# Performance work log

Hardware: AMD Instinct MI355X
Metric: run time of the kernel (lower is better)

## Reference

```python
import jax, jax.numpy as jnp
import numpy as np

D_MODEL = 1024
N_HEADS = 16
HEAD_DIM = D_MODEL // N_HEADS


def setup_inputs() -> dict:
    key = jax.random.key(0)
    ks = jax.random.split(key, 5)
    B, T = 4, 2048
    x = jax.random.normal(ks[0], (B, T, D_MODEL), dtype=jnp.float32)
    s_in = 1.0 / np.sqrt(D_MODEL)
    W_qkv = jax.random.normal(ks[1], (D_MODEL, 3 * D_MODEL), dtype=jnp.float32) * s_in
    b_qkv = jnp.zeros((3 * D_MODEL,), dtype=jnp.float32)
    W_proj = jax.random.normal(ks[2], (D_MODEL, D_MODEL), dtype=jnp.float32) * s_in
    b_proj = jnp.zeros((D_MODEL,), dtype=jnp.float32)
    return {"x": x, "W_qkv": W_qkv, "b_qkv": b_qkv, "W_proj": W_proj, "b_proj": b_proj}


def reference(x, W_qkv, b_qkv, W_proj, b_proj):
    B, T, C = x.shape
    qkv = x @ W_qkv + b_qkv                       # [B, T, 3C]
    q, k, v = jnp.split(qkv, 3, axis=-1)
    def heads(t):  # [B, T, C] -> [B, H, T, Dh]
        return t.reshape(B, T, N_HEADS, HEAD_DIM).transpose(0, 2, 1, 3)
    q, k, v = heads(q), heads(k), heads(v)
    scale = 1.0 / np.sqrt(HEAD_DIM)
    att = jnp.einsum('bhqd,bhkd->bhqk', q, k) * scale   # [B, H, T, T]
    causal = jnp.tril(jnp.ones((T, T), dtype=bool))
    att = jnp.where(causal, att, -jnp.inf)
    att = jax.nn.softmax(att, axis=-1)
    out = jnp.einsum('bhqk,bhkd->bhqd', att, v)          # [B, H, T, Dh]
    out = out.transpose(0, 2, 1, 3).reshape(B, T, C)
    return out @ W_proj + b_proj
```

## Files before the change

kernel.cpp:

```cpp
#include <hip/hip_runtime.h>
#include <hip/hip_bf16.h>

#define NH 16
#define HD 64
#define T_SEQ 2048
#define DM 1024

typedef __attribute__((ext_vector_type(8))) short short8;
typedef __attribute__((ext_vector_type(4))) short sh4;
typedef __attribute__((ext_vector_type(4))) float f32x4;
typedef __attribute__((ext_vector_type(16))) float f32x16;
typedef unsigned short ushort;

static __device__ __forceinline__ ushort f2bf(float f) {
    union { float f; unsigned int u; } c; c.f = f;
    unsigned int r = (c.u + 0x7fffu + ((c.u >> 16) & 1u)) >> 16;
    return (ushort)r;
}

static __device__ __forceinline__ void gload16(const ushort* g, ushort* l) {
    __builtin_amdgcn_global_load_lds(
        (const __attribute__((address_space(1))) void*)(const void*)g,
        (__attribute__((address_space(3))) void*)(void*)l, 16, 0, 0);
}

__global__ __launch_bounds__(256) void prep(const float* __restrict__ X,
                                            ushort* __restrict__ Xb,
                                            const float* __restrict__ W,
                                            ushort* __restrict__ Wt) {
    __shared__ float Ts[64][65];
    const int tid = threadIdx.x;
    if (blockIdx.x < 4096) {
        int i = blockIdx.x * 256 + tid;
        const float* s = X + (size_t)i * 8;
        float4 a = *(const float4*)(s);
        float4 b = *(const float4*)(s + 4);
        short8 o;
        o[0] = f2bf(a.x); o[1] = f2bf(a.y); o[2] = f2bf(a.z); o[3] = f2bf(a.w);
        o[4] = f2bf(b.x); o[5] = f2bf(b.y); o[6] = f2bf(b.z); o[7] = f2bf(b.w);
        *(short8*)(Xb + (size_t)i * 8) = o;
    } else {
        const int bid = blockIdx.x - 4096;
        const int N = 3 * DM;
        const int n0 = (bid % 48) * 64, k0 = (bid / 48) * 64;
        const int cg = tid & 15, r4 = tid >> 4;
        #pragma unroll
        for (int i = 0; i < 4; ++i) {
            int r = r4 + i * 16;
            float4 v = *(const float4*)(W + (size_t)(k0 + r) * N + n0 + cg * 4);
            Ts[r][cg * 4 + 0] = v.x; Ts[r][cg * 4 + 1] = v.y;
            Ts[r][cg * 4 + 2] = v.z; Ts[r][cg * 4 + 3] = v.w;
        }
        __syncthreads();
        #pragma unroll
        for (int i = 0; i < 4; ++i) {
            int r = r4 + i * 16;
            sh4 o;
            o[0] = (short)f2bf(Ts[cg * 4 + 0][r]);
            o[1] = (short)f2bf(Ts[cg * 4 + 1][r]);
            o[2] = (short)f2bf(Ts[cg * 4 + 2][r]);
            o[3] = (short)f2bf(Ts[cg * 4 + 3][r]);
            *(sh4*)(Wt + (size_t)(n0 + r) * DM + k0 + cg * 4) = o;
        }
    }
}

__global__ __launch_bounds__(256) void transpose_w(const float* __restrict__ W,
                                                   ushort* __restrict__ Wt, int N) {
    __shared__ float Ts[64][65];
    const int n0 = blockIdx.x * 64, k0 = blockIdx.y * 64;
    const int tid = threadIdx.x;
    const int cg = tid & 15, r4 = tid >> 4;
    #pragma unroll
    for (int i = 0; i < 4; ++i) {
        int r = r4 + i * 16;
        float4 v = *(const float4*)(W + (size_t)(k0 + r) * N + n0 + cg * 4);
        Ts[r][cg * 4 + 0] = v.x; Ts[r][cg * 4 + 1] = v.y;
        Ts[r][cg * 4 + 2] = v.z; Ts[r][cg * 4 + 3] = v.w;
    }
    __syncthreads();
    #pragma unroll
    for (int i = 0; i < 4; ++i) {
        int r = r4 + i * 16;
        sh4 o;
        o[0] = (short)f2bf(Ts[cg * 4 + 0][r]);
        o[1] = (short)f2bf(Ts[cg * 4 + 1][r]);
        o[2] = (short)f2bf(Ts[cg * 4 + 2][r]);
        o[3] = (short)f2bf(Ts[cg * 4 + 3][r]);
        *(sh4*)(Wt + (size_t)(n0 + r) * DM + k0 + cg * 4) = o;
    }
}

static __device__ __forceinline__ void gemm_core(
    const ushort* __restrict__ A, const ushort* __restrict__ Bt,
    ushort* __restrict__ smem, int m0, int n0, f32x4 acc[4][4])
{
    const int tid = threadIdx.x;
    const int wid = tid >> 6, lane = tid & 63;
    const int lr = lane & 15, g = lane >> 4;
    const int wm = wid >> 1, wn = wid & 1;
    const int lrow = lane >> 3, lslot = lane & 7;

    auto stage = [&](int b, int kt) {
        ushort* As = smem + b * 16384;
        ushort* Bs = As + 8192;
        #pragma unroll
        for (int i = 0; i < 4; ++i) {
            const int row = wid * 32 + i * 8 + lrow;
            const int gcol = (lslot ^ (row & 7)) * 8;
            const int ldsoff = (wid * 32 + i * 8) * 64;
            gload16(A  + (size_t)(m0 + row) * DM + kt * 64 + gcol, As + ldsoff);
            gload16(Bt + (size_t)(n0 + row) * DM + kt * 64 + gcol, Bs + ldsoff);
        }
    };

    stage(0, 0);
    #pragma unroll 1
    for (int kt = 0; kt < 16; ++kt) {
        const int cur = kt & 1;
        if (kt < 15) {
            stage(cur ^ 1, kt + 1);
            asm volatile("s_waitcnt vmcnt(8)" ::: "memory");
        } else {
            asm volatile("s_waitcnt vmcnt(0)" ::: "memory");
        }
        __builtin_amdgcn_s_barrier();
        __builtin_amdgcn_sched_barrier(0);
        const ushort* As = smem + cur * 16384;
        const ushort* Bs = As + 8192;
        #pragma unroll
        for (int ks = 0; ks < 2; ++ks) {
            short8 af[4], bfr[4];
            #pragma unroll
            for (int mi = 0; mi < 4; ++mi) {
                int row = wm * 64 + mi * 16 + lr;
                af[mi] = *(const short8*)(As + row * 64 + (((ks * 4 + g) ^ (row & 7)) * 8));
            }
            #pragma unroll
            for (int ni = 0; ni < 4; ++ni) {
                int row = wn * 64 + ni * 16 + lr;
                bfr[ni] = *(const short8*)(Bs + row * 64 + (((ks * 4 + g) ^ (row & 7)) * 8));
            }
            #pragma unroll
            for (int mi = 0; mi < 4; ++mi)
                #pragma unroll
                for (int ni = 0; ni < 4; ++ni)
                    acc[mi][ni] = __builtin_amdgcn_mfma_f32_16x16x32_bf16(af[mi], bfr[ni], acc[mi][ni], 0, 0, 0);
        }
        __builtin_amdgcn_sched_barrier(0);
        __builtin_amdgcn_s_barrier();
    }
}

__global__ __launch_bounds__(256) void qkv_mfma(
    const ushort* __restrict__ Xb, const ushort* __restrict__ Wqt,
    const float* __restrict__ bias,
    ushort* __restrict__ Qb, ushort* __restrict__ Kb, ushort* __restrict__ Vt)
{
    __shared__ __align__(16) ushort smem[32768];
    const int m0 = blockIdx.y * 128;
    const int n0 = blockIdx.x * 128;
    f32x4 acc[4][4] = {};
    gemm_core(Xb, Wqt, smem, m0, n0, acc);

    const int tid = threadIdx.x;
    const int wid = tid >> 6, lane = tid & 63;
    const int lr = lane & 15, g = lane >> 4;
    const int wm = wid >> 1, wn = wid & 1;
    const int which = n0 >> 10;
    const int bq = m0 >> 11;

    if (which < 2) {
        ushort* dst = which ? Kb : Qb;
        const float sc = which ? 1.0f : 0.125f * 1.44269504f;
        #pragma unroll
        for (int ni = 0; ni < 4; ++ni) {
            int nn = n0 + wn * 64 + ni * 16 + lr;
            const float bv = bias[nn];
            const int hh = (nn & 1023) >> 6, dd = nn & 63;
            const size_t hb = ((size_t)(bq * NH + hh)) * T_SEQ;
            #pragma unroll
            for (int mi = 0; mi < 4; ++mi)
                #pragma unroll
                for (int r = 0; r < 4; ++r) {
                    int t = (m0 + wm * 64 + mi * 16 + g * 4 + r) & 2047;
                    dst[(hb + t) * HD + dd] = f2bf((acc[mi][ni][r] + bv) * sc);
                }
        }
    } else {
        __syncthreads();
        ushort* Ct = smem;
        #pragma unroll
        for (int ni = 0; ni < 4; ++ni) {
            int lcol = wn * 64 + ni * 16 + lr;
            const float bv = bias[n0 + lcol];
            #pragma unroll
            for (int mi = 0; mi < 4; ++mi)
                #pragma unroll
                for (int r = 0; r < 4; ++r)
                    Ct[(wm * 64 + mi * 16 + g * 4 + r) * 128 + lcol] = f2bf(acc[mi][ni][r] + bv);
        }
        __syncthreads();
        const int dloc = tid >> 1, th = (tid & 1) * 64;
        const int nn = (n0 & 1023) + dloc;
        ushort* dst = Vt + ((size_t)(bq * 1024 + nn)) * T_SEQ + (m0 & 2047) + th;
        #pragma unroll
        for (int e8 = 0; e8 < 8; ++e8) {
            short8 v;
            #pragma unroll
            for (int u = 0; u < 8; ++u) v[u] = (short)Ct[(th + e8 * 8 + u) * 128 + dloc];
            *(short8*)(dst + e8 * 8) = v;
        }
    }
}

__global__ __launch_bounds__(256) void proj_mfma(
    const ushort* __restrict__ AO, const ushort* __restrict__ Wpt,
    const float* __restrict__ bias, float* __restrict__ Y)
{
    __shared__ __align__(16) ushort smem[32768];
    const int m0 = blockIdx.y * 128;
    const int n0 = blockIdx.x * 128;
    f32x4 acc[4][4] = {};
    gemm_core(AO, Wpt, smem, m0, n0, acc);

    const int tid = threadIdx.x;
    const int wid = tid >> 6, lane = tid & 63;
    const int lr = lane & 15, g = lane >> 4;
    const int wm = wid >> 1, wn = wid & 1;
    #pragma unroll
    for (int ni = 0; ni < 4; ++ni) {
        int nn = n0 + wn * 64 + ni * 16 + lr;
        const float bv = bias[nn];
        #pragma unroll
        for (int mi = 0; mi < 4; ++mi)
            #pragma unroll
            for (int r = 0; r < 4; ++r) {
                int m = m0 + wm * 64 + mi * 16 + g * 4 + r;
                Y[(size_t)m * DM + nn] = acc[mi][ni][r] + bv;
            }
    }
}

__global__ __launch_bounds__(256) void attn_mfma(
    const ushort* __restrict__ Qb,
    const ushort* __restrict__ Kb,
    const ushort* __restrict__ Vt,
    ushort* __restrict__ AO)
{
    __shared__ __align__(16) ushort Ks[2][4096];
    __shared__ __align__(16) ushort Vs[2][4096];

    const int bh = blockIdx.x;
    const int j = 15 - blockIdx.y;
    const int tid = threadIdx.x;
    const int wid = tid >> 6;
    const int lane = tid & 63;
    const int ql = lane & 31;
    const int hi = lane >> 5;

    const ushort* Kg = Kb + (size_t)bh * T_SEQ * HD;
    const ushort* Vg = Vt + (size_t)bh * HD * T_SEQ;

    const int srow = tid >> 3;
    const int sco = (tid & 7) * 8;
    const int ssw = sco ^ ((srow & 7) << 3);
    const int sdst0 = srow * 64 + ssw;
    const int sdst1 = (srow + 32) * 64 + ssw;

    const int b = bh >> 4, h = bh & 15;
    ushort* AOg = AO + (size_t)b * T_SEQ * DM + h * HD;

    const int q0 = j * 128;
    const int qlo = q0 + wid * 32;
    const int ntiles = 2 * j + 2;

    short8 qb[4];
    {
        const ushort* Qg = Qb + ((size_t)bh * T_SEQ + qlo) * HD;
        #pragma unroll
        for (int ds = 0; ds < 4; ++ds)
            qb[ds] = *(const short8*)(Qg + (size_t)ql * HD + ds * 16 + hi * 8);
    }

    f32x16 po[2] = {};
    float lp = 0.f;

    short8 rk0, rk1, rv0, rv1;
    rk0 = *(const short8*)(Kg + (size_t)srow * HD + sco);
    rk1 = *(const short8*)(Kg + (size_t)(srow + 32) * HD + sco);
    rv0 = *(const short8*)(Vg + (size_t)srow * T_SEQ + sco);
    rv1 = *(const short8*)(Vg + (size_t)(srow + 32) * T_SEQ + sco);
    *(short8*)(&Ks[0][sdst0]) = rk0;  *(short8*)(&Ks[0][sdst1]) = rk1;
    *(short8*)(&Vs[0][sdst0]) = rv0;  *(short8*)(&Vs[0][sdst1]) = rv1;
    {
        const int nk0 = 64;
        rk0 = *(const short8*)(Kg + (size_t)(nk0 + srow) * HD + sco);
        rk1 = *(const short8*)(Kg + (size_t)(nk0 + srow + 32) * HD + sco);
        rv0 = *(const short8*)(Vg + (size_t)srow * T_SEQ + nk0 + sco);
        rv1 = *(const short8*)(Vg + (size_t)(srow + 32) * T_SEQ + nk0 + sco);
    }
    __syncthreads();

    for (int tt = 0; tt < ntiles; ++tt) {
        const int k0 = tt * 64;
        const int cur = tt & 1;
        if (tt + 1 < ntiles) {
            const int nxt = cur ^ 1;
            *(short8*)(&Ks[nxt][sdst0]) = rk0;  *(short8*)(&Ks[nxt][sdst1]) = rk1;
            *(short8*)(&Vs[nxt][sdst0]) = rv0;  *(short8*)(&Vs[nxt][sdst1]) = rv1;
            if (tt + 2 < ntiles) {
                const int nk0 = (tt + 2) * 64;
                rk0 = *(const short8*)(Kg + (size_t)(nk0 + srow) * HD + sco);
                rk1 = *(const short8*)(Kg + (size_t)(nk0 + srow + 32) * HD + sco);
                rv0 = *(const short8*)(Vg + (size_t)srow * T_SEQ + nk0 + sco);
                rv1 = *(const short8*)(Vg + (size_t)(srow + 32) * T_SEQ + nk0 + sco);
            }
        }

        if (k0 <= qlo + 31) {
            const ushort* ksb = Ks[cur];
            const ushort* vsb = Vs[cur];

            short8 vf[2][4];
            #pragma unroll
            for (int db = 0; db < 2; ++db)
                #pragma unroll
                for (int sl = 0; sl < 4; ++sl) {
                    int row = db * 32 + ql;
                    int slot = (sl * 2 + hi) ^ (row & 7);
                    vf[db][sl] = *(const short8*)(&vsb[row * 64 + slot * 8]);
                }

            f32x16 sp[2] = {};
            __builtin_amdgcn_s_setprio(1);
            #pragma unroll
            for (int kb = 0; kb < 2; ++kb) {
                #pragma unroll
                for (int ds = 0; ds < 4; ++ds) {
                    int row = kb * 32 + ql;
                    int slot = (ds * 2 + hi) ^ (row & 7);
                    short8 kf = *(const short8*)(&ksb[row * 64 + slot * 8]);
                    sp[kb] = __builtin_amdgcn_mfma_f32_32x32x16_bf16(kf, qb[ds], sp[kb], 0, 0, 0);
                }
            }
            __builtin_amdgcn_s_setprio(0);

            if (k0 + 63 > qlo) {
                #pragma unroll
                for (int kb = 0; kb < 2; ++kb) {
                    const int lim = qlo + ql - k0 - kb * 32 - 4 * hi;
                    #pragma unroll
                    for (int r = 0; r < 16; ++r) {
                        const int c = (r & 3) + 8 * (r >> 2);
                        sp[kb][r] = (c <= lim) ? sp[kb][r] : -INFINITY;
                    }
                }
            }

            float rs = 0.f;
            #pragma unroll
            for (int kb = 0; kb < 2; ++kb)
                #pragma unroll
                for (int r = 0; r < 16; ++r) {
                    float p;
                    asm("v_exp_f32 %0, %1" : "=v"(p) : "v"(sp[kb][r]));
                    sp[kb][r] = p;
                    rs += p;
                }
            lp += rs;

            #pragma unroll
            for (int kb = 0; kb < 2; ++kb) {
                #pragma unroll
                for (int ks16 = 0; ks16 < 2; ++ks16) {
                    unsigned int x0, x1, y0, y1;
                    const int rb0 = ks16 * 2, rb1 = ks16 * 2 + 1;
                    asm("v_cvt_pk_bf16_f32 %0, %1, %2" : "=v"(x0)
                        : "v"(sp[kb][4 * rb0 + 0]), "v"(sp[kb][4 * rb0 + 1]));
                    asm("v_cvt_pk_bf16_f32 %0, %1, %2" : "=v"(x1)
                        : "v"(sp[kb][4 * rb0 + 2]), "v"(sp[kb][4 * rb0 + 3]));
                    asm("v_cvt_pk_bf16_f32 %0, %1, %2" : "=v"(y0)
                        : "v"(sp[kb][4 * rb1 + 0]), "v"(sp[kb][4 * rb1 + 1]));
                    asm("v_cvt_pk_bf16_f32 %0, %1, %2" : "=v"(y1)
                        : "v"(sp[kb][4 * rb1 + 2]), "v"(sp[kb][4 * rb1 + 3]));
                    asm("v_permlane32_swap_b32 %0, %1" : "+v"(x0), "+v"(y0));
                    asm("v_permlane32_swap_b32 %0, %1" : "+v"(x1), "+v"(y1));
                    union { unsigned int w[4]; short8 s8; } pb;
                    pb.w[0] = x0; pb.w[1] = x1; pb.w[2] = y0; pb.w[3] = y1;
                    const int sl = kb * 2 + ks16;
                    __builtin_amdgcn_s_setprio(1);
                    po[0] = __builtin_amdgcn_mfma_f32_32x32x16_bf16(vf[0][sl], pb.s8, po[0], 0, 0, 0);
                    po[1] = __builtin_amdgcn_mfma_f32_32x32x16_bf16(vf[1][sl], pb.s8, po[1], 0, 0, 0);
                    __builtin_amdgcn_s_setprio(0);
                }
            }
        }
        __syncthreads();
    }

    lp += __shfl_xor(lp, 32);
    const float inv = 1.f / lp;
    const int q = qlo + ql;
    #pragma unroll
    for (int db = 0; db < 2; ++db) {
        #pragma unroll
        for (int rb = 0; rb < 4; ++rb) {
            unsigned int w0, w1;
            float f0 = po[db][4 * rb + 0] * inv, f1 = po[db][4 * rb + 1] * inv;
            float f2 = po[db][4 * rb + 2] * inv, f3 = po[db][4 * rb + 3] * inv;
            asm("v_cvt_pk_bf16_f32 %0, %1, %2" : "=v"(w0) : "v"(f0), "v"(f1));
            asm("v_cvt_pk_bf16_f32 %0, %1, %2" : "=v"(w1) : "v"(f2), "v"(f3));
            uint2 wv; wv.x = w0; wv.y = w1;
            *(uint2*)(AOg + (size_t)q * DM + db * 32 + 8 * rb + 4 * hi) = wv;
        }
    }
}

extern "C" void kernel_launch(void* const* d_in, const int* in_sizes, int n_in,
                              void* d_out, int out_size, void* d_ws, size_t ws_size,
                              hipStream_t stream) {
    const float* x      = (const float*)d_in[0];
    const float* W_qkv  = (const float*)d_in[1];
    const float* b_qkv  = (const float*)d_in[2];
    const float* W_proj = (const float*)d_in[3];
    const float* b_proj = (const float*)d_in[4];
    float* out = (float*)d_out;

    const size_t perbuf = (size_t)4 * NH * T_SEQ * HD;
    ushort* Qb  = (ushort*)d_ws;
    ushort* Kb  = Qb + perbuf;
    ushort* Vt  = Kb + perbuf;
    ushort* AO  = Vt + perbuf;
    ushort* Wqt = AO;
    ushort* Wpt = Qb;
    ushort* Xb  = (ushort*)d_out;

    hipLaunchKernelGGL(prep, dim3(4096 + 768), dim3(256), 0, stream, x, Xb, W_qkv, Wqt);
    hipLaunchKernelGGL(qkv_mfma, dim3(24, 64), dim3(256), 0, stream,
                       Xb, Wqt, b_qkv, Qb, Kb, Vt);
    hipLaunchKernelGGL(attn_mfma, dim3(64, 16), dim3(256), 0, stream,
                       Qb, Kb, Vt, AO);
    hipLaunchKernelGGL(transpose_w, dim3(16, 16), dim3(256), 0, stream, W_proj, Wpt, DM);
    hipLaunchKernelGGL(proj_mfma, dim3(8, 64), dim3(256), 0, stream,
                       AO, Wpt, b_proj, out);
}
```

Baseline: 158.5 us.

## Stage K/V tiles with direct global-to-LDS loads and vmcnt-based double buffering

Replaces the register-staged K/V prefetch (global load into registers, then an LDS store) with global_load_lds 16-byte direct copies into the double-buffered shared tiles, swizzled per 8-row group. Synchronisation becomes explicit s_waitcnt vmcnt plus s_barrier, with sched_barrier fences around the compute region. The goal is to free the VGPRs that held prefetched tiles and drop the LDS store instructions. In exchange, prefetch depth shrinks from two tiles ahead to one, and correctness depends on the vmcnt counts and the swizzle matching the read pattern.

```diff
diff --git a/kernel.cpp b/kernel.cpp
--- a/kernel.cpp
+++ b/kernel.cpp
@@ -262,12 +262,6 @@
     const ushort* Kg = Kb + (size_t)bh * T_SEQ * HD;
     const ushort* Vg = Vt + (size_t)bh * HD * T_SEQ;
 
-    const int srow = tid >> 3;
-    const int sco = (tid & 7) * 8;
-    const int ssw = sco ^ ((srow & 7) << 3);
-    const int sdst0 = srow * 64 + ssw;
-    const int sdst1 = (srow + 32) * 64 + ssw;
-
     const int b = bh >> 4, h = bh & 15;
     ushort* AOg = AO + (size_t)b * T_SEQ * DM + h * HD;
 
@@ -275,6 +269,9 @@
     const int qlo = q0 + wid * 32;
     const int ntiles = 2 * j + 2;
 
+    const int lrow8 = lane >> 3;
+    const int gsl = ((lane & 7) ^ lrow8) * 8;
+
     short8 qb[4];
     {
         const ushort* Qg = Qb + ((size_t)bh * T_SEQ + qlo) * HD;
@@ -286,37 +283,34 @@
     f32x16 po[2] = {};
     float lp = 0.f;
 
-    short8 rk0, rk1, rv0, rv1;
-    rk0 = *(const short8*)(Kg + (size_t)srow * HD + sco);
-    rk1 = *(const short8*)(Kg + (size_t)(srow + 32) * HD + sco);
-    rv0 = *(const short8*)(Vg + (size_t)srow * T_SEQ + sco);
-    rv1 = *(const short8*)(Vg + (size_t)(srow + 32) * T_SEQ + sco);
-    *(short8*)(&Ks[0][sdst0]) = rk0;  *(short8*)(&Ks[0][sdst1]) = rk1;
-    *(short8*)(&Vs[0][sdst0]) = rv0;  *(short8*)(&Vs[0][sdst1]) = rv1;
-    {
-        const int nk0 = 64;
-        rk0 = *(const short8*)(Kg + (size_t)(nk0 + srow) * HD + sco);
-        rk1 = *(const short8*)(Kg + (size_t)(nk0 + srow + 32) * HD + sco);
-        rv0 = *(const short8*)(Vg + (size_t)srow * T_SEQ + nk0 + sco);
-        rv1 = *(const short8*)(Vg + (size_t)(srow + 32) * T_SEQ + nk0 + sco);
-    }
-    __syncthreads();
+    auto stage = [&](int buf, int tts) {
+        const int k0s = tts * 64;
+        #pragma unroll
+        for (int i = 0; i < 4; ++i) {
+            const int s = wid * 4 + i;
+            if (s < 8) {
+                const int row = s * 8 + lrow8;
+                gload16(Kg + (size_t)(k0s + row) * HD + gsl, &Ks[buf][s * 512]);
+            } else {
+                const int row = (s - 8) * 8 + lrow8;
+                gload16(Vg + (size_t)row * T_SEQ + k0s + gsl, &Vs[buf][(s - 8) * 512]);
+            }
+        }
+    };
+
+    stage(0, 0);
 
     for (int tt = 0; tt < ntiles; ++tt) {
         const int k0 = tt * 64;
         const int cur = tt & 1;
         if (tt + 1 < ntiles) {
-            const int nxt = cur ^ 1;
-            *(short8*)(&Ks[nxt][sdst0]) = rk0;  *(short8*)(&Ks[nxt][sdst1]) = rk1;
-            *(short8*)(&Vs[nxt][sdst0]) = rv0;  *(short8*)(&Vs[nxt][sdst1]) = rv1;
-            if (tt + 2 < ntiles) {
-                const int nk0 = (tt + 2) * 64;
-                rk0 = *(const short8*)(Kg + (size_t)(nk0 + srow) * HD + sco);
-                rk1 = *(const short8*)(Kg + (size_t)(nk0 + srow + 32) * HD + sco);
-                rv0 = *(const short8*)(Vg + (size_t)srow * T_SEQ + nk0 + sco);
-                rv1 = *(const short8*)(Vg + (size_t)(srow + 32) * T_SEQ + nk0 + sco);
-            }
-        }
+            stage(cur ^ 1, tt + 1);
+            asm volatile("s_waitcnt vmcnt(4)" ::: "memory");
+        } else {
+            asm volatile("s_waitcnt vmcnt(0)" ::: "memory");
+        }
+        __builtin_amdgcn_s_barrier();
+        __builtin_amdgcn_sched_barrier(0);
 
         if (k0 <= qlo + 31) {
             const ushort* ksb = Ks[cur];
@@ -396,7 +390,8 @@
                 }
             }
         }
-        __syncthreads();
+        __builtin_amdgcn_sched_barrier(0);
+        __builtin_amdgcn_s_barrier();
     }
 
     lp += __shfl_xor(lp, 32);
```

New measurement: 162.3 us. +2.4%, slower.
